# Kernel optimization log

Hardware: AMD Instinct MI355X
Metric: run time of the kernel (lower is better)

## Reference

```python
import jax, jax.numpy as jnp
from jax import lax
import numpy as np

B, C, Hf, Wf = 4, 256, 64, 64
COMP = max(C // 4, 16)  # 64
SCALE, K_UP, K_ENC = 2, 5, 3
EPS = 1e-5


def setup_inputs() -> dict:
    key = jax.random.key(0)
    ks = jax.random.split(key, 6)
    x = jax.random.normal(ks[0], (B, C, Hf, Wf), dtype=jnp.float32)
    w_comp = jax.random.normal(ks[1], (COMP, C), dtype=jnp.float32) * (1.0 / np.sqrt(C))
    bn_gamma = jnp.ones((COMP,), dtype=jnp.float32)
    bn_beta = jnp.zeros((COMP,), dtype=jnp.float32)
    bn_mean = jax.random.normal(ks[2], (COMP,), dtype=jnp.float32) * 0.1
    bn_var = jax.random.uniform(ks[3], (COMP,), dtype=jnp.float32, minval=0.5, maxval=1.5)
    w_enc = jax.random.normal(ks[4], (K_UP * K_UP * SCALE * SCALE, COMP, K_ENC, K_ENC), dtype=jnp.float32) * (1.0 / np.sqrt(COMP * K_ENC * K_ENC))
    return {"x": x, "w_comp": w_comp, "bn_gamma": bn_gamma, "bn_beta": bn_beta,
            "bn_mean": bn_mean, "bn_var": bn_var, "w_enc": w_enc}


def reference(x, w_comp, bn_gamma, bn_beta, bn_mean, bn_var, w_enc):
    b, c, h, w = x.shape
    s, k = SCALE, K_UP
    # 1x1 compression conv
    comp = jnp.einsum('bchw,oc->bohw', x, w_comp)
    # BatchNorm (eval-style, running stats) + SiLU
    inv = (bn_gamma / jnp.sqrt(bn_var + EPS))[:, None, None]
    bn = (comp - bn_mean[:, None, None]) * inv + bn_beta[:, None, None]
    act = bn * jax.nn.sigmoid(bn)
    # encoder conv -> per-pixel reassembly kernels, channels = k^2 * s^2 (k2 outer, s2 inner)
    mask = lax.conv_general_dilated(act, w_enc, (1, 1), ((1, 1), (1, 1)),
                                    dimension_numbers=('NCHW', 'OIHW', 'NCHW'))
    mask = mask.reshape(b, k * k, s * s, h, w)
    mask = jax.nn.softmax(mask, axis=1)  # softmax over k_up*k_up window
    # unfold: gather 5x5 neighborhoods (pad 2), k = dy*5+dx row-major like F.unfold
    pad = k // 2
    xp = jnp.pad(x, ((0, 0), (0, 0), (pad, pad), (pad, pad)))
    patches = jnp.stack([xp[:, :, dy:dy + h, dx:dx + w]
                         for dy in range(k) for dx in range(k)], axis=2)  # (b,c,k2,h,w)
    # content-aware weighted sum per sub-pixel position
    out = jnp.einsum('bksij,bckij->bcsij', mask, patches)  # (b,c,s2,h,w)
    # s2 -> (s0,s1); pixel (i*s+s0, j*s+s1)
    out = out.reshape(b, c, s, s, h, w).transpose(0, 1, 4, 2, 5, 3).reshape(b, c, h * s, w * s)
    return out
```

## Files before the change

### kernel.cpp

```cpp
#include <hip/hip_runtime.h>
#include <hip/hip_bf16.h>
#include <hip/hip_fp16.h>
#include <math.h>

#define B_ 4
#define C_ 256
#define H_ 64
#define W_ 64
#define COMP_ 64
#define K2_ 25
#define HW_ (H_*W_)
#define EPS_ 1e-5f

typedef float v2f __attribute__((ext_vector_type(2)));
typedef float f32x4 __attribute__((ext_vector_type(4)));
typedef _Float16 half8 __attribute__((ext_vector_type(8)));
#define FMA2(a, b, c) __builtin_elementwise_fma((a), (b), (c))

__global__ void k_transpose(const float* __restrict__ w_comp,
                            const float* __restrict__ w_enc,
                            float* __restrict__ wTc,
                            __half* __restrict__ Apack) {
    int t = blockIdx.x * 256 + threadIdx.x;
    if (t < COMP_ * C_) {
        int o = t & 63;
        int c = t >> 6;
        wTc[t] = w_comp[o * C_ + c];
    } else {
        int t2 = t - COMP_ * C_;
        if (t2 < 8 * 18 * 64) {
            int lane = t2 & 63;
            int ks   = (t2 >> 6) % 18;
            int MT   = t2 / (64 * 18);
            int m    = MT * 16 + (lane & 15);
            __half vals[8];
#pragma unroll
            for (int e = 0; e < 8; ++e) {
                int k = ks * 32 + (lane >> 4) * 8 + e;
                int q = k >> 6;
                int c = k & 63;
                float wv = (m < 100) ? w_enc[(m * COMP_ + c) * 9 + q] : 0.f;
                vals[e] = __float2half(wv);
            }
            *(float4*)&Apack[(size_t)t2 * 8] = *(float4*)vals;
        }
    }
}

__global__ void __launch_bounds__(512)
k_compress(const float* __restrict__ x, const float* __restrict__ wTc,
           const float* __restrict__ gamma, const float* __restrict__ beta,
           const float* __restrict__ mean, const float* __restrict__ var,
           __half* __restrict__ act16) {
    __shared__ float sx[256 * 68];
    const int tx = threadIdx.x;
    const int ty = threadIdx.y;
    const int tid = ty * 64 + tx;
    const int ogu = __builtin_amdgcn_readfirstlane(ty);
    const int bb = blockIdx.y;
    const int p0 = blockIdx.x * 64;

    const float* xb = x + (size_t)bb * C_ * HW_ + p0;
#pragma unroll
    for (int l = 0; l < 8; ++l) {
        int e = tid + l * 512;
        int c = e >> 4;
        int p4 = (e & 15) << 2;
        float4 v4 = *(const float4*)(xb + (size_t)c * HW_ + p4);
        *(float4*)&sx[c * 68 + p4] = v4;
    }
    __syncthreads();

    v2f acc2[4];
#pragma unroll
    for (int k = 0; k < 4; ++k) acc2[k] = (v2f){0.f, 0.f};

#pragma unroll 8
    for (int c = 0; c < 256; ++c) {
        float xv = sx[c * 68 + tx];
        const v2f* w2 = (const v2f*)(wTc + c * COMP_ + ogu * 8);
        v2f xv2 = (v2f){xv, xv};
#pragma unroll
        for (int k = 0; k < 4; ++k)
            acc2[k] = FMA2(xv2, w2[k], acc2[k]);
    }

    __half h8[8];
#pragma unroll
    for (int k = 0; k < 4; ++k) {
#pragma unroll
        for (int h = 0; h < 2; ++h) {
            int o = ty * 8 + 2 * k + h;
            float sv = (h == 0) ? acc2[k].x : acc2[k].y;
            float iv = gamma[o] * rsqrtf(var[o] + EPS_);
            float bn = (sv - mean[o]) * iv + beta[o];
            float sg = 1.f / (1.f + __expf(-bn));
            h8[2 * k + h] = __float2half(bn * sg);
        }
    }
    __syncthreads();
    __half* sxh = (__half*)sx;
    *(float2*)&sxh[tx * 68 + ty * 8]     = *(float2*)&h8[0];
    *(float2*)&sxh[tx * 68 + ty * 8 + 4] = *(float2*)&h8[4];
    __syncthreads();

    {
        int px = tid >> 3, c8 = tid & 7;
        float2 alo = *(float2*)&sxh[px * 68 + c8 * 8];
        float2 ahi = *(float2*)&sxh[px * 68 + c8 * 8 + 4];
        float4 v = make_float4(alo.x, alo.y, ahi.x, ahi.y);
        __half* ao = act16 + ((size_t)bb * HW_ + p0 + px) * COMP_ + c8 * 8;
        *(float4*)ao = v;
    }
}

__global__ void __launch_bounds__(512)
k_encoder(const __half* __restrict__ act16, const __half* __restrict__ Apack,
          __half* __restrict__ maskT) {
    __shared__ __align__(16) __half sact[3 * 34 * 80];
    __shared__ float cbuf[32 * 129];
    __shared__ __align__(16) __half st[32 * 100];
    const int tid = threadIdx.x;
    const int i = blockIdx.x, b = blockIdx.y, jh = blockIdx.z;
    const int lane = tid & 63, w = tid >> 6;

    const __half* ab = act16 + (size_t)b * HW_ * COMP_;
    for (int t = tid; t < 3 * 34 * 8; t += 512) {
        int c8 = t & 7;
        int s  = (t >> 3) % 34;
        int r  = t / (34 * 8);
        int gi = i + r - 1;
        int gj = jh * 32 + s - 1;
        float4 v = make_float4(0.f, 0.f, 0.f, 0.f);
        if ((unsigned)gi < 64u && (unsigned)gj < 64u)
            v = *(const float4*)(ab + ((size_t)gi * 64 + gj) * COMP_ + c8 * 8);
        *(float4*)((char*)sact + (size_t)(r * 34 + s) * 160 + c8 * 16) = v;
    }
    __syncthreads();

    const int jloc0 = (w & 1) * 16;
    const int MT0   = (w >> 1) * 2;
    const int p = lane & 15, g = lane >> 4;
    f32x4 acc[2];
#pragma unroll
    for (int mt = 0; mt < 2; ++mt) acc[mt] = (f32x4){0.f, 0.f, 0.f, 0.f};
    const half8* Ap = (const half8*)Apack;
#pragma unroll
    for (int ks = 0; ks < 18; ++ks) {
        const int q = ks >> 1, ky = q / 3, kx = q % 3;
        half8 bf = *(const half8*)((const char*)sact +
                       (size_t)(ky * 34 + jloc0 + p + kx) * 160 +
                       ((ks & 1) * 32 + g * 8) * 2);
#pragma unroll
        for (int mt = 0; mt < 2; ++mt) {
            half8 af = Ap[((size_t)(MT0 + mt) * 18 + ks) * 64 + lane];
            acc[mt] = __builtin_amdgcn_mfma_f32_16x16x32_f16(af, bf, acc[mt], 0, 0, 0);
        }
    }

#pragma unroll
    for (int mt = 0; mt < 2; ++mt)
#pragma unroll
        for (int r4 = 0; r4 < 4; ++r4)
            cbuf[(jloc0 + p) * 129 + (MT0 + mt) * 16 + g * 4 + r4] = acc[mt][r4];
    __syncthreads();

    if (tid < 128) {
        int px = tid & 31, s2 = tid >> 5;
        float v[K2_];
        float mx = -1e30f;
#pragma unroll
        for (int k2 = 0; k2 < K2_; ++k2) {
            v[k2] = cbuf[px * 129 + k2 * 4 + s2];
            mx = fmaxf(mx, v[k2]);
        }
        float sum = 0.f;
#pragma unroll
        for (int k2 = 0; k2 < K2_; ++k2) { v[k2] = __expf(v[k2] - mx); sum += v[k2]; }
        float rs = 1.f / sum;
#pragma unroll
        for (int k2 = 0; k2 < K2_; ++k2)
            st[px * 100 + k2 * 4 + s2] = __float2half(v[k2] * rs);
    }
    __syncthreads();

    float4* dst = (float4*)(maskT + ((size_t)b * HW_ + i * 64 + jh * 32) * 100);
    const float4* src = (const float4*)st;
    if (tid < 400) dst[tid] = src[tid];
}

__global__ void __launch_bounds__(512)
k_reassemble(const float* __restrict__ x, const __half* __restrict__ maskT,
             float* __restrict__ out) {
    __shared__ float maskF[K2_ * 256];
    __shared__ float sx[2][5 * 68 * 20];
    const int tx = threadIdx.x;
    const int ty = threadIdx.y;
    const int tid = ty * 64 + tx;

    const int bid = blockIdx.x;
    const int id  = ((bid & 7) << 6) | (bid >> 3);
    const int half = id & 1;
    const int i    = (id >> 1) & 63;
    const int b    = id >> 7;
    const int cc0  = half * 8;

    float4 vx[3];
    int offs[3];
    auto LOADX = [&](int cc) {
#pragma unroll
        for (int l = 0; l < 3; ++l) {
            int e = tid + l * 512;
            int q = e / 340;
            int rem = e - q * 340;
            int r = rem / 68;
            int col = rem - r * 68;
            int gi = i + r - 2;
            int gj = col - 2;
            offs[l] = (r * 68 + col) * 20 + q * 4;
            float4 v = make_float4(0.f, 0.f, 0.f, 0.f);
            if (e < 1360 && (unsigned)gi < 64u && (unsigned)gj < 64u) {
                const float* p = x + ((size_t)b * C_ + cc * 16 + q * 4) * HW_ + gi * W_ + gj;
                v.x = p[0];
                v.y = p[HW_];
                v.z = p[2 * HW_];
                v.w = p[3 * HW_];
            }
            vx[l] = v;
        }
    };
    auto WRITEX = [&](int d) {
#pragma unroll
        for (int l = 0; l < 3; ++l) {
            int e = tid + l * 512;
            if (e < 1360) *(float4*)&sx[d][offs[l]] = vx[l];
        }
    };

    LOADX(cc0);
    {
        const __half* mrow = maskT + ((size_t)b * HW_ + i * 64) * 100;
#pragma unroll
        for (int t = 0; t < 4; ++t) {
            int f = tid + t * 512;
            if (f < 1600) {
                float2 raw = *(const float2*)(mrow + f * 4);
                __half2 lo = ((const __half2*)&raw)[0];
                __half2 hi = ((const __half2*)&raw)[1];
                float2 flo = __half22float2(lo);
                float2 fhi = __half22float2(hi);
                int px = f / 25, k2 = f - px * 25;
                *(float4*)&maskF[k2 * 256 + px * 4] =
                    make_float4(flo.x, flo.y, fhi.x, fhi.y);
            }
        }
    }
    WRITEX(0);
    __syncthreads();

    int dbuf = 0;
#pragma unroll 1
    for (int n = 0; n < 8; ++n) {
        const int cc = cc0 + n;
        if (n < 7) LOADX(cc + 1);

        const float* sb = sx[dbuf];
        v2f a01[2], a23[2];
#pragma unroll
        for (int cl = 0; cl < 2; ++cl) { a01[cl] = (v2f){0.f, 0.f}; a23[cl] = (v2f){0.f, 0.f}; }

        float4 mq = *(const float4*)&maskF[tx * 4];
        float2 xv = *(const float2*)&sb[(0 * 68 + tx + 0) * 20 + ty * 2];
#pragma unroll
        for (int k2 = 0; k2 < K2_; ++k2) {
            float4 mq_c = mq;
            float2 xv_c = xv;
            if (k2 < K2_ - 1) {
                const int kn = k2 + 1;
                const int dy = kn / 5, dx = kn % 5;
                mq = *(const float4*)&maskF[kn * 256 + tx * 4];
                xv = *(const float2*)&sb[(dy * 68 + tx + dx) * 20 + ty * 2];
            }
            v2f m01 = (v2f){mq_c.x, mq_c.y};
            v2f m23 = (v2f){mq_c.z, mq_c.w};
            float xc[2] = {xv_c.x, xv_c.y};
#pragma unroll
            for (int cl = 0; cl < 2; ++cl) {
                v2f xv2 = (v2f){xc[cl], xc[cl]};
                a01[cl] = FMA2(xv2, m01, a01[cl]);
                a23[cl] = FMA2(xv2, m23, a23[cl]);
            }
        }

        if (n < 7) WRITEX(dbuf ^ 1);

#pragma unroll
        for (int cl = 0; cl < 2; ++cl) {
            int c = cc * 16 + ty * 2 + cl;
            float* op = out + (((size_t)(b * C_ + c) * 128 + 2 * i) * 128) + 2 * tx;
            *(float2*)op         = float2{a01[cl].x, a01[cl].y};
            *(float2*)(op + 128) = float2{a23[cl].x, a23[cl].y};
        }

        if (n < 7) __syncthreads();
        dbuf ^= 1;
    }
}

extern "C" void kernel_launch(void* const* d_in, const int* in_sizes, int n_in,
                              void* d_out, int out_size, void* d_ws, size_t ws_size,
                              hipStream_t stream) {
    const float* x       = (const float*)d_in[0];
    const float* w_comp  = (const float*)d_in[1];
    const float* bn_g    = (const float*)d_in[2];
    const float* bn_b    = (const float*)d_in[3];
    const float* bn_m    = (const float*)d_in[4];
    const float* bn_v    = (const float*)d_in[5];
    const float* w_enc   = (const float*)d_in[6];
    float* out = (float*)d_out;

    float* ws     = (float*)d_ws;
    float* wTc    = ws;
    __half* Apack = (__half*)(ws + 16384);
    __half* act16 = (__half*)(ws + 53248);
    __half* maskT = (__half*)(ws + 577536);

    k_transpose<<<100, 256, 0, stream>>>(w_comp, w_enc, wTc, Apack);
    k_compress<<<dim3(64, B_), dim3(64, 8), 0, stream>>>(x, wTc, bn_g, bn_b, bn_m, bn_v, act16);
    k_encoder<<<dim3(64, B_, 2), 512, 0, stream>>>(act16, Apack, maskT);
    k_reassemble<<<512, dim3(64, 8), 0, stream>>>(x, maskT, out);
}
```

Baseline: 148.1 us.

## Hold reassembly mask weights in registers and drop the separate mask shared buffer

```diff
diff --git a/kernel.cpp b/kernel.cpp
--- a/kernel.cpp
+++ b/kernel.cpp
@@ -189,14 +189,15 @@
     if (tid < 400) dst[tid] = src[tid];
 }
 
-__global__ void __launch_bounds__(512)
+__global__ void __launch_bounds__(512, 4)
 k_reassemble(const float* __restrict__ x, const __half* __restrict__ maskT,
              float* __restrict__ out) {
-    __shared__ float maskF[K2_ * 256];
     __shared__ float sx[2][5 * 68 * 20];
     const int tx = threadIdx.x;
     const int ty = threadIdx.y;
     const int tid = ty * 64 + tx;
+    const int s2p = ty & 1;
+    const int chq = ty >> 1;
 
     const int bid = blockIdx.x;
     const int id  = ((bid & 7) << 6) | (bid >> 3);
@@ -205,22 +206,30 @@
     const int b    = id >> 7;
     const int cc0  = half * 8;
 
+    int    offs[3];
+    size_t goff[3];
+    bool   vld[3];
+#pragma unroll
+    for (int l = 0; l < 3; ++l) {
+        int e = tid + l * 512;
+        int q = e / 340;
+        int rem = e - q * 340;
+        int r = rem / 68;
+        int col = rem - r * 68;
+        int gi = i + r - 2;
+        int gj = col - 2;
+        offs[l] = (r * 68 + col) * 20 + q * 4;
+        vld[l]  = (e < 1360) && ((unsigned)gi < 64u) && ((unsigned)gj < 64u);
+        goff[l] = (size_t)(q * 4) * HW_ + (size_t)gi * W_ + gj;
+    }
     float4 vx[3];
-    int offs[3];
     auto LOADX = [&](int cc) {
+        const float* xit = x + ((size_t)b * C_ + cc * 16) * HW_;
 #pragma unroll
         for (int l = 0; l < 3; ++l) {
-            int e = tid + l * 512;
-            int q = e / 340;
-            int rem = e - q * 340;
-            int r = rem / 68;
-            int col = rem - r * 68;
-            int gi = i + r - 2;
-            int gj = col - 2;
-            offs[l] = (r * 68 + col) * 20 + q * 4;
             float4 v = make_float4(0.f, 0.f, 0.f, 0.f);
-            if (e < 1360 && (unsigned)gi < 64u && (unsigned)gj < 64u) {
-                const float* p = x + ((size_t)b * C_ + cc * 16 + q * 4) * HW_ + gi * W_ + gj;
+            if (vld[l]) {
+                const float* p = xit + goff[l];
                 v.x = p[0];
                 v.y = p[HW_];
                 v.z = p[2 * HW_];
@@ -238,6 +247,8 @@
     };
 
     LOADX(cc0);
+
+    float* mbuf = &sx[1][0];
     {
         const __half* mrow = maskT + ((size_t)b * HW_ + i * 64) * 100;
 #pragma unroll
@@ -250,11 +261,19 @@
                 float2 flo = __half22float2(lo);
                 float2 fhi = __half22float2(hi);
                 int px = f / 25, k2 = f - px * 25;
-                *(float4*)&maskF[k2 * 256 + px * 4] =
+                *(float4*)&mbuf[k2 * 256 + px * 4] =
                     make_float4(flo.x, flo.y, fhi.x, fhi.y);
             }
         }
     }
+    __syncthreads();
+
+    v2f mreg[K2_];
+#pragma unroll
+    for (int k2 = 0; k2 < K2_; ++k2)
+        mreg[k2] = *(const v2f*)&mbuf[k2 * 256 + tx * 4 + s2p * 2];
+    __syncthreads();
+
     WRITEX(0);
     __syncthreads();
 
@@ -265,41 +284,35 @@
         if (n < 7) LOADX(cc + 1);
 
         const float* sb = sx[dbuf];
-        v2f a01[2], a23[2];
-#pragma unroll
-        for (int cl = 0; cl < 2; ++cl) { a01[cl] = (v2f){0.f, 0.f}; a23[cl] = (v2f){0.f, 0.f}; }
-
-        float4 mq = *(const float4*)&maskF[tx * 4];
-        float2 xv = *(const float2*)&sb[(0 * 68 + tx + 0) * 20 + ty * 2];
+        v2f acc[4];
+#pragma unroll
+        for (int cl = 0; cl < 4; ++cl) acc[cl] = (v2f){0.f, 0.f};
+
+        float4 xq = *(const float4*)&sb[(0 * 68 + tx + 0) * 20 + chq * 4];
 #pragma unroll
         for (int k2 = 0; k2 < K2_; ++k2) {
-            float4 mq_c = mq;
-            float2 xv_c = xv;
+            float4 xq_c = xq;
             if (k2 < K2_ - 1) {
                 const int kn = k2 + 1;
                 const int dy = kn / 5, dx = kn % 5;
-                mq = *(const float4*)&maskF[kn * 256 + tx * 4];
-                xv = *(const float2*)&sb[(dy * 68 + tx + dx) * 20 + ty * 2];
-            }
-            v2f m01 = (v2f){mq_c.x, mq_c.y};
-            v2f m23 = (v2f){mq_c.z, mq_c.w};
-            float xc[2] = {xv_c.x, xv_c.y};
-#pragma unroll
-            for (int cl = 0; cl < 2; ++cl) {
+                xq = *(const float4*)&sb[(dy * 68 + tx + dx) * 20 + chq * 4];
+            }
+            v2f m = mreg[k2];
+            float xc[4] = {xq_c.x, xq_c.y, xq_c.z, xq_c.w};
+#pragma unroll
+            for (int cl = 0; cl < 4; ++cl) {
                 v2f xv2 = (v2f){xc[cl], xc[cl]};
-                a01[cl] = FMA2(xv2, m01, a01[cl]);
-                a23[cl] = FMA2(xv2, m23, a23[cl]);
+                acc[cl] = FMA2(xv2, m, acc[cl]);
             }
         }
 
         if (n < 7) WRITEX(dbuf ^ 1);
 
 #pragma unroll
-        for (int cl = 0; cl < 2; ++cl) {
-            int c = cc * 16 + ty * 2 + cl;
-            float* op = out + (((size_t)(b * C_ + c) * 128 + 2 * i) * 128) + 2 * tx;
-            *(float2*)op         = float2{a01[cl].x, a01[cl].y};
-            *(float2*)(op + 128) = float2{a23[cl].x, a23[cl].y};
+        for (int cl = 0; cl < 4; ++cl) {
+            int c = cc * 16 + chq * 4 + cl;
+            float* op = out + (((size_t)(b * C_ + c) * 128 + 2 * i + s2p) * 128) + 2 * tx;
+            *(float2*)op = float2{acc[cl].x, acc[cl].y};
         }
 
         if (n < 7) __syncthreads();
```

After: 207.1 us. +39.9%, slower.
